# Kernel tuning notes

Hardware: AMD Instinct MI355X
Metric: run time of the kernel (lower is better)

The kernel has to match this reference:

```python
import jax, jax.numpy as jnp
import numpy as np

MARGIN = 200.0
EPS = 1e-6  # torch F.pairwise_distance default eps (added to the difference)


def setup_inputs() -> dict:
    key = jax.random.key(0)
    k1, k2, k3 = jax.random.split(key, 3)
    B2, T, D = 128, 1024, 1024  # 2*batch_size, snippets, feature dim
    scores = jax.random.normal(k1, (B2, T), dtype=jnp.float32)
    feats = jax.random.normal(k2, (B2, T, D), dtype=jnp.float32)
    targets = jax.random.uniform(k3, (B2, T), dtype=jnp.float32)
    return {"scores": scores, "feats": feats, "targets": targets}


def _bce_with_logits(logits, targets):
    # mean over all elements of max(x,0) - x*t + log(1+exp(-|x|))
    return jnp.mean(jnp.maximum(logits, 0.0) - logits * targets
                    + jnp.log1p(jnp.exp(-jnp.abs(logits))))


def _contrastive(M):
    # M: [2b, T] feature magnitudes (L1 norms). Split into normal / abnormal.
    b = M.shape[0] // 2
    n_f, a_f = M[:b], M[b:]
    # pairwise euclidean distance d_ij = ||n_i - a_j + eps||_2   [b, b]
    diff = n_f[:, None, :] - a_f[None, :, :] + EPS
    dist = jnp.sqrt(jnp.sum(diff * diff, axis=-1))
    d = jnp.square(jnp.maximum(MARGIN - dist, 0.0))
    # strict '<' in the torch loop => first flat occurrence of the min
    flat_idx = jnp.argmin(d.reshape(-1))
    i_star = flat_idx // b
    j_star = flat_idx % b
    min_d = d.reshape(-1)[flat_idx]
    loss_con = 0.001 * min_d
    # loss_n: sum_{i != i*} ||n_i - n_{i*} + eps||^2 / b
    dn = n_f - n_f[i_star] + EPS
    sq_n = jnp.sum(dn * dn, axis=-1)          # [b]
    loss_n = (jnp.sum(sq_n) - sq_n[i_star]) / b
    da = a_f - a_f[j_star] + EPS
    sq_a = jnp.sum(da * da, axis=-1)
    loss_a = (jnp.sum(sq_a) - sq_a[j_star]) / b
    return loss_con + loss_n + loss_a


def reference(scores, feats, targets):
    loss_cls = _bce_with_logits(scores, targets)
    mags = jnp.sum(jnp.abs(feats), axis=2)    # torch.norm(p=1, dim=2) -> [2b, T]
    loss_con = _contrastive(mags)
    return loss_cls + 0.001 * loss_con
```

## Files before the change

kernel.cpp:

```cpp
#include <hip/hip_runtime.h>
#include <math.h>

#define NB2   128
#define NT    1024
#define ND    1024
#define BHALF 64
#define NROWS (NB2 * NT)
#define MARGIN_F 200.0f
#define EPS_F    1e-6f


__device__ __forceinline__ float wave_reduce_sum(float s) {
#pragma unroll
    for (int off = 32; off > 0; off >>= 1)
        s += __shfl_xor(s, off, 64);
    return s;
}

__global__ void mags_kernel(const float* __restrict__ feats,
                            float* __restrict__ mags) {
    const int wave = threadIdx.x >> 6;
    const int lane = threadIdx.x & 63;
    const int row  = blockIdx.x * 4 + wave;
    const float* src = feats + (size_t)row * ND;
    float s = 0.0f;
#pragma unroll
    for (int it = 0; it < 4; ++it) {
        float4 v = *reinterpret_cast<const float4*>(src + lane * 4 + it * 256);
        s += fabsf(v.x) + fabsf(v.y) + fabsf(v.z) + fabsf(v.w);
    }
    s = wave_reduce_sum(s);
    if (lane == 0) mags[row] = s;
}

__global__ void bce_kernel(const float* __restrict__ scores,
                           const float* __restrict__ targets,
                           float* __restrict__ ws) {
    const int idx = blockIdx.x * blockDim.x + threadIdx.x;
    float4 l4 = reinterpret_cast<const float4*>(scores)[idx];
    float4 t4 = reinterpret_cast<const float4*>(targets)[idx];
    float s = 0.0f;
    {
        float l = l4.x, t = t4.x;
        s += fmaxf(l, 0.0f) - l * t + log1pf(expf(-fabsf(l)));
        l = l4.y; t = t4.y;
        s += fmaxf(l, 0.0f) - l * t + log1pf(expf(-fabsf(l)));
        l = l4.z; t = t4.z;
        s += fmaxf(l, 0.0f) - l * t + log1pf(expf(-fabsf(l)));
        l = l4.w; t = t4.w;
        s += fmaxf(l, 0.0f) - l * t + log1pf(expf(-fabsf(l)));
    }
    s = wave_reduce_sum(s);
    __shared__ float lds[4];
    const int wave = threadIdx.x >> 6;
    const int lane = threadIdx.x & 63;
    if (lane == 0) lds[wave] = s;
    __syncthreads();
    if (threadIdx.x == 0) {
        float b = lds[0] + lds[1] + lds[2] + lds[3];
        atomicAdd(&ws[0], b);
    }
}

__global__ void dist_kernel(const float* __restrict__ mags,
                            float* __restrict__ dmat) {
    const int wave = threadIdx.x >> 6;
    const int lane = threadIdx.x & 63;
    const int pair = blockIdx.x * 4 + wave;
    const int i = pair >> 6;
    const int j = pair & 63;
    const float* nf = mags + (size_t)i * NT;
    const float* af = mags + (size_t)(BHALF + j) * NT;
    float s = 0.0f;
#pragma unroll
    for (int it = 0; it < 4; ++it) {
        float4 a = *reinterpret_cast<const float4*>(nf + lane * 4 + it * 256);
        float4 b = *reinterpret_cast<const float4*>(af + lane * 4 + it * 256);
        float dx = a.x - b.x + EPS_F; s += dx * dx;
        dx = a.y - b.y + EPS_F; s += dx * dx;
        dx = a.z - b.z + EPS_F; s += dx * dx;
        dx = a.w - b.w + EPS_F; s += dx * dx;
    }
    s = wave_reduce_sum(s);
    if (lane == 0) {
        float dist = sqrtf(s);
        float m = MARGIN_F - dist;
        dmat[pair] = (m > 0.0f) ? m * m : 0.0f;
    }
}

__global__ void argmin_kernel(const float* __restrict__ dmat,
                              float* __restrict__ ws) {
    __shared__ float sv[256];
    __shared__ int   si[256];
    const int t = threadIdx.x;
    float best = INFINITY;
    int   bidx = 0x7FFFFFFF;
    for (int k = t; k < 4096; k += 256) {
        float v = dmat[k];
        if (v < best || (v == best && k < bidx)) { best = v; bidx = k; }
    }
    sv[t] = best; si[t] = bidx;
    __syncthreads();
    for (int s = 128; s > 0; s >>= 1) {
        if (t < s) {
            float v2 = sv[t + s]; int i2 = si[t + s];
            if (v2 < sv[t] || (v2 == sv[t] && i2 < si[t])) { sv[t] = v2; si[t] = i2; }
        }
        __syncthreads();
    }
    if (t == 0) {
        ws[3] = sv[0];
        int* wsi = reinterpret_cast<int*>(ws);
        wsi[4] = si[0] >> 6;
        wsi[5] = si[0] & 63;
    }
}

__global__ void lossna_kernel(const float* __restrict__ mags,
                              float* __restrict__ ws) {
    const int gwave = (blockIdx.x * blockDim.x + threadIdx.x) >> 6;
    const int lane  = threadIdx.x & 63;
    const int* wsi  = reinterpret_cast<const int*>(ws);
    const int istar = wsi[4];
    const int jstar = wsi[5];

    int row, ref, accslot;
    if (gwave < BHALF) {
        row = gwave; ref = istar; accslot = 1;
        if (row == istar) return;
    } else {
        row = gwave; ref = BHALF + jstar; accslot = 2;
        if (gwave - BHALF == jstar) return;
    }
    const float* r0 = mags + (size_t)row * NT;
    const float* r1 = mags + (size_t)ref * NT;
    float s = 0.0f;
#pragma unroll
    for (int it = 0; it < 4; ++it) {
        float4 a = *reinterpret_cast<const float4*>(r0 + lane * 4 + it * 256);
        float4 b = *reinterpret_cast<const float4*>(r1 + lane * 4 + it * 256);
        float dx = a.x - b.x + EPS_F; s += dx * dx;
        dx = a.y - b.y + EPS_F; s += dx * dx;
        dx = a.z - b.z + EPS_F; s += dx * dx;
        dx = a.w - b.w + EPS_F; s += dx * dx;
    }
    s = wave_reduce_sum(s);
    if (lane == 0) atomicAdd(&ws[accslot], s);
}

__global__ void finalize_kernel(const float* __restrict__ ws,
                                float* __restrict__ out) {
    float bce    = ws[0] / (float)NROWS;
    float loss_c = 0.001f * ws[3];
    float loss_n = ws[1] / (float)BHALF;
    float loss_a = ws[2] / (float)BHALF;
    out[0] = bce + 0.001f * (loss_c + loss_n + loss_a);
}

extern "C" void kernel_launch(void* const* d_in, const int* in_sizes, int n_in,
                              void* d_out, int out_size, void* d_ws, size_t ws_size,
                              hipStream_t stream) {
    const float* scores  = (const float*)d_in[0];
    const float* feats   = (const float*)d_in[1];
    const float* targets = (const float*)d_in[2];
    float* out  = (float*)d_out;
    float* ws   = (float*)d_ws;
    float* dmat = ws + 8;
    float* mags = ws + 8192;

    hipMemsetAsync(d_ws, 0, 32, stream);

    mags_kernel  <<<NROWS / 4, 256, 0, stream>>>(feats, mags);
    bce_kernel   <<<NROWS / 4 / 256, 256, 0, stream>>>(scores, targets, ws);
    dist_kernel  <<<4096 / 4, 256, 0, stream>>>(mags, dmat);
    argmin_kernel<<<1, 256, 0, stream>>>(dmat, ws);
    lossna_kernel<<<128 * 64 / 256, 256, 0, stream>>>(mags, ws);
    finalize_kernel<<<1, 1, 0, stream>>>(ws, out);
}
```

Measured before the change: 117.8 us.

## Fuse BCE into mags kernel and merge argmin, loss terms and finalize

```diff
diff --git a/kernel.cpp b/kernel.cpp
--- a/kernel.cpp
+++ b/kernel.cpp
@@ -1,5 +1,7 @@
 #include <hip/hip_runtime.h>
 #include <math.h>
+
+typedef float f32x4 __attribute__((ext_vector_type(4)));
 
 #define NB2   128
 #define NT    1024
@@ -9,6 +11,9 @@
 #define MARGIN_F 200.0f
 #define EPS_F    1e-6f
 
+#define MAGS_BLOCKS (NROWS / 4)
+#define BCE_BLOCKS  128
+
 
 __device__ __forceinline__ float wave_reduce_sum(float s) {
 #pragma unroll
@@ -17,49 +22,45 @@
     return s;
 }
 
-__global__ void mags_kernel(const float* __restrict__ feats,
-                            float* __restrict__ mags) {
+__global__ void mags_bce_kernel(const float* __restrict__ feats,
+                                const float* __restrict__ scores,
+                                const float* __restrict__ targets,
+                                float* __restrict__ mags,
+                                float* __restrict__ bce_part) {
     const int wave = threadIdx.x >> 6;
     const int lane = threadIdx.x & 63;
-    const int row  = blockIdx.x * 4 + wave;
-    const float* src = feats + (size_t)row * ND;
+
+    if (blockIdx.x < MAGS_BLOCKS) {
+        const int row = blockIdx.x * 4 + wave;
+        const float* src = feats + (size_t)row * ND;
+        float s = 0.0f;
+#pragma unroll
+        for (int it = 0; it < 4; ++it) {
+            f32x4 v = __builtin_nontemporal_load(
+                reinterpret_cast<const f32x4*>(src + lane * 4 + it * 256));
+            s += fabsf(v.x) + fabsf(v.y) + fabsf(v.z) + fabsf(v.w);
+        }
+        s = wave_reduce_sum(s);
+        if (lane == 0) mags[row] = s;
+        return;
+    }
+
+    const int b   = blockIdx.x - MAGS_BLOCKS;
+    const int idx = b * 256 + threadIdx.x;
+    f32x4 l4 = reinterpret_cast<const f32x4*>(scores)[idx];
+    f32x4 t4 = reinterpret_cast<const f32x4*>(targets)[idx];
     float s = 0.0f;
 #pragma unroll
-    for (int it = 0; it < 4; ++it) {
-        float4 v = *reinterpret_cast<const float4*>(src + lane * 4 + it * 256);
-        s += fabsf(v.x) + fabsf(v.y) + fabsf(v.z) + fabsf(v.w);
-    }
-    s = wave_reduce_sum(s);
-    if (lane == 0) mags[row] = s;
-}
-
-__global__ void bce_kernel(const float* __restrict__ scores,
-                           const float* __restrict__ targets,
-                           float* __restrict__ ws) {
-    const int idx = blockIdx.x * blockDim.x + threadIdx.x;
-    float4 l4 = reinterpret_cast<const float4*>(scores)[idx];
-    float4 t4 = reinterpret_cast<const float4*>(targets)[idx];
-    float s = 0.0f;
-    {
-        float l = l4.x, t = t4.x;
-        s += fmaxf(l, 0.0f) - l * t + log1pf(expf(-fabsf(l)));
-        l = l4.y; t = t4.y;
-        s += fmaxf(l, 0.0f) - l * t + log1pf(expf(-fabsf(l)));
-        l = l4.z; t = t4.z;
-        s += fmaxf(l, 0.0f) - l * t + log1pf(expf(-fabsf(l)));
-        l = l4.w; t = t4.w;
+    for (int c = 0; c < 4; ++c) {
+        float l = l4[c], t = t4[c];
         s += fmaxf(l, 0.0f) - l * t + log1pf(expf(-fabsf(l)));
     }
     s = wave_reduce_sum(s);
     __shared__ float lds[4];
-    const int wave = threadIdx.x >> 6;
-    const int lane = threadIdx.x & 63;
     if (lane == 0) lds[wave] = s;
     __syncthreads();
-    if (threadIdx.x == 0) {
-        float b = lds[0] + lds[1] + lds[2] + lds[3];
-        atomicAdd(&ws[0], b);
-    }
+    if (threadIdx.x == 0)
+        bce_part[b] = lds[0] + lds[1] + lds[2] + lds[3];
 }
 
 __global__ void dist_kernel(const float* __restrict__ mags,
@@ -74,12 +75,13 @@
     float s = 0.0f;
 #pragma unroll
     for (int it = 0; it < 4; ++it) {
-        float4 a = *reinterpret_cast<const float4*>(nf + lane * 4 + it * 256);
-        float4 b = *reinterpret_cast<const float4*>(af + lane * 4 + it * 256);
-        float dx = a.x - b.x + EPS_F; s += dx * dx;
-        dx = a.y - b.y + EPS_F; s += dx * dx;
-        dx = a.z - b.z + EPS_F; s += dx * dx;
-        dx = a.w - b.w + EPS_F; s += dx * dx;
+        f32x4 a = *reinterpret_cast<const f32x4*>(nf + lane * 4 + it * 256);
+        f32x4 b = *reinterpret_cast<const f32x4*>(af + lane * 4 + it * 256);
+#pragma unroll
+        for (int c = 0; c < 4; ++c) {
+            float dx = a[c] - b[c] + EPS_F;
+            s += dx * dx;
+        }
     }
     s = wave_reduce_sum(s);
     if (lane == 0) {
@@ -89,73 +91,90 @@
     }
 }
 
-__global__ void argmin_kernel(const float* __restrict__ dmat,
-                              float* __restrict__ ws) {
-    __shared__ float sv[256];
-    __shared__ int   si[256];
-    const int t = threadIdx.x;
+__global__ void __launch_bounds__(1024)
+mega_kernel(const float* __restrict__ mags,
+            const float* __restrict__ dmat,
+            const float* __restrict__ bce_part,
+            float* __restrict__ out) {
+    __shared__ float sval[16];
+    __shared__ int   sidx[16];
+    __shared__ float bpart2[2];
+    __shared__ float partials[16];
+    __shared__ float s_mind;
+    __shared__ int   s_istar, s_jstar;
+    __shared__ float s_bce;
+
+    const int t    = threadIdx.x;
+    const int wave = t >> 6;
+    const int lane = t & 63;
+
     float best = INFINITY;
     int   bidx = 0x7FFFFFFF;
-    for (int k = t; k < 4096; k += 256) {
+#pragma unroll
+    for (int k = t; k < 4096; k += 1024) {
         float v = dmat[k];
         if (v < best || (v == best && k < bidx)) { best = v; bidx = k; }
     }
-    sv[t] = best; si[t] = bidx;
+#pragma unroll
+    for (int off = 32; off > 0; off >>= 1) {
+        float v2 = __shfl_xor(best, off, 64);
+        int   i2 = __shfl_xor(bidx, off, 64);
+        if (v2 < best || (v2 == best && i2 < bidx)) { best = v2; bidx = i2; }
+    }
+    if (lane == 0) { sval[wave] = best; sidx[wave] = bidx; }
+
+    if (t < 128) {
+        float s = wave_reduce_sum(bce_part[t]);
+        if (lane == 0) bpart2[wave] = s;
+    }
     __syncthreads();
-    for (int s = 128; s > 0; s >>= 1) {
-        if (t < s) {
-            float v2 = sv[t + s]; int i2 = si[t + s];
-            if (v2 < sv[t] || (v2 == sv[t] && i2 < si[t])) { sv[t] = v2; si[t] = i2; }
-        }
-        __syncthreads();
+
+    if (t == 0) {
+        float bv = sval[0]; int bi = sidx[0];
+        for (int w = 1; w < 16; ++w)
+            if (sval[w] < bv || (sval[w] == bv && sidx[w] < bi)) { bv = sval[w]; bi = sidx[w]; }
+        s_mind  = bv;
+        s_istar = bi >> 6;
+        s_jstar = bi & 63;
+        s_bce   = bpart2[0] + bpart2[1];
     }
-    if (t == 0) {
-        ws[3] = sv[0];
-        int* wsi = reinterpret_cast<int*>(ws);
-        wsi[4] = si[0] >> 6;
-        wsi[5] = si[0] & 63;
-    }
-}
+    __syncthreads();
 
-__global__ void lossna_kernel(const float* __restrict__ mags,
-                              float* __restrict__ ws) {
-    const int gwave = (blockIdx.x * blockDim.x + threadIdx.x) >> 6;
-    const int lane  = threadIdx.x & 63;
-    const int* wsi  = reinterpret_cast<const int*>(ws);
-    const int istar = wsi[4];
-    const int jstar = wsi[5];
+    const int  istar = s_istar, jstar = s_jstar;
+    const bool is_a  = (wave >= 8);
+    const int  row0  = is_a ? (BHALF + (wave - 8) * 8) : (wave * 8);
+    const int  ref   = is_a ? (BHALF + jstar) : istar;
+    const float* r1  = mags + (size_t)ref * NT;
 
-    int row, ref, accslot;
-    if (gwave < BHALF) {
-        row = gwave; ref = istar; accslot = 1;
-        if (row == istar) return;
-    } else {
-        row = gwave; ref = BHALF + jstar; accslot = 2;
-        if (gwave - BHALF == jstar) return;
-    }
-    const float* r0 = mags + (size_t)row * NT;
-    const float* r1 = mags + (size_t)ref * NT;
     float s = 0.0f;
 #pragma unroll
-    for (int it = 0; it < 4; ++it) {
-        float4 a = *reinterpret_cast<const float4*>(r0 + lane * 4 + it * 256);
-        float4 b = *reinterpret_cast<const float4*>(r1 + lane * 4 + it * 256);
-        float dx = a.x - b.x + EPS_F; s += dx * dx;
-        dx = a.y - b.y + EPS_F; s += dx * dx;
-        dx = a.z - b.z + EPS_F; s += dx * dx;
-        dx = a.w - b.w + EPS_F; s += dx * dx;
+    for (int r = 0; r < 8; ++r) {
+        const int row = row0 + r;
+        if (row == ref) continue;
+        const float* r0 = mags + (size_t)row * NT;
+#pragma unroll
+        for (int it = 0; it < 4; ++it) {
+            f32x4 a = *reinterpret_cast<const f32x4*>(r0 + lane * 4 + it * 256);
+            f32x4 b = *reinterpret_cast<const f32x4*>(r1 + lane * 4 + it * 256);
+#pragma unroll
+            for (int c = 0; c < 4; ++c) {
+                float dx = a[c] - b[c] + EPS_F;
+                s += dx * dx;
+            }
+        }
     }
     s = wave_reduce_sum(s);
-    if (lane == 0) atomicAdd(&ws[accslot], s);
-}
+    if (lane == 0) partials[wave] = s;
+    __syncthreads();
 
-__global__ void finalize_kernel(const float* __restrict__ ws,
-                                float* __restrict__ out) {
-    float bce    = ws[0] / (float)NROWS;
-    float loss_c = 0.001f * ws[3];
-    float loss_n = ws[1] / (float)BHALF;
-    float loss_a = ws[2] / (float)BHALF;
-    out[0] = bce + 0.001f * (loss_c + loss_n + loss_a);
+    if (t == 0) {
+        float ln = 0.0f, la = 0.0f;
+        for (int w = 0; w < 8; ++w)  ln += partials[w];
+        for (int w = 8; w < 16; ++w) la += partials[w];
+        float bce      = s_bce / (float)NROWS;
+        float contrast = 0.001f * s_mind + ln / (float)BHALF + la / (float)BHALF;
+        out[0] = bce + 0.001f * contrast;
+    }
 }
 
 extern "C" void kernel_launch(void* const* d_in, const int* in_sizes, int n_in,
@@ -164,17 +183,14 @@
     const float* scores  = (const float*)d_in[0];
     const float* feats   = (const float*)d_in[1];
     const float* targets = (const float*)d_in[2];
-    float* out  = (float*)d_out;
-    float* ws   = (float*)d_ws;
-    float* dmat = ws + 8;
-    float* mags = ws + 8192;
+    float* out      = (float*)d_out;
+    float* ws       = (float*)d_ws;
+    float* bce_part = ws + 64;
+    float* dmat     = ws + 1024;
+    float* mags     = ws + 8192;
 
-    hipMemsetAsync(d_ws, 0, 32, stream);
-
-    mags_kernel  <<<NROWS / 4, 256, 0, stream>>>(feats, mags);
-    bce_kernel   <<<NROWS / 4 / 256, 256, 0, stream>>>(scores, targets, ws);
-    dist_kernel  <<<4096 / 4, 256, 0, stream>>>(mags, dmat);
-    argmin_kernel<<<1, 256, 0, stream>>>(dmat, ws);
-    lossna_kernel<<<128 * 64 / 256, 256, 0, stream>>>(mags, ws);
-    finalize_kernel<<<1, 1, 0, stream>>>(ws, out);
+    mags_bce_kernel<<<MAGS_BLOCKS + BCE_BLOCKS, 256, 0, stream>>>(
+        feats, scores, targets, mags, bce_part);
+    dist_kernel<<<4096 / 4, 256, 0, stream>>>(mags, dmat);
+    mega_kernel<<<1, 1024, 0, stream>>>(mags, dmat, bce_part, out);
 }
```

Measured after the change: 98.29 us. 16.6% less time.
